# Optimization experiments

Measured on AMD Instinct MI355X. Metric: run time of the kernel, lower is better.

## Reference

```python
import jax, jax.numpy as jnp
import numpy as np

NUM_TOKENS = 8192
HIDDEN = 4096
NUM_EXPERTS = 64
TOP_K = 8


def setup_inputs() -> dict:
    key = jax.random.key(0)
    k1, k2, k3 = jax.random.split(key, 3)
    tokens = jax.random.normal(k1, (NUM_TOKENS, HIDDEN), dtype=jnp.float32)
    token_probs = jax.random.uniform(k2, (NUM_TOKENS, NUM_EXPERTS), dtype=jnp.float32)
    # exactly TOP_K experts per token -> static num_out_tokens
    scores = jax.random.normal(k3, (NUM_TOKENS, NUM_EXPERTS))
    _, topk_idx = jax.lax.top_k(scores, TOP_K)  # [T, K]
    rows = jnp.arange(NUM_TOKENS)[:, None]
    routing_map = jnp.zeros((NUM_TOKENS, NUM_EXPERTS), dtype=bool).at[rows, topk_idx].set(True)
    return {
        "tokens": tokens,
        "token_probs": token_probs,
        "routing_map": routing_map,
        "num_out_tokens": NUM_TOKENS * TOP_K,
    }


def reference(tokens, token_probs, routing_map, num_out_tokens):
    # Fallback (non-fused) path of TurboTokenPermuter.forward.
    num_tokens, _ = tokens.shape
    # routing_map.bool().T -> [E, T]; masked_select in row-major order =
    # for each expert (in order), the token ids routed to it (in token order).
    flat_mask = routing_map.T.reshape(-1)  # [E*T]
    # stable argsort of ~mask puts flat positions of True entries first, in order
    perm = jnp.argsort(~flat_mask, stable=True)[:num_out_tokens]  # flat E*T indices
    sorted_indices = (perm % num_tokens).astype(jnp.int32)  # token ids (column index)
    permuted_probs = token_probs.T.reshape(-1)[perm]
    permuted_input = tokens[sorted_indices]  # index_select along dim 0
    return permuted_input, permuted_probs, sorted_indices
```

## Files before the change

kernel.cpp:

```cpp
#include <hip/hip_runtime.h>
#include <stdint.h>

#define NTOK   8192
#define NEXP   64
#define HID    4096
#define TOPK   8
#define OUTROW 65536
#define CHUNK  256
#define NCHUNK (NTOK / CHUNK)
#define NPART  (NEXP * NCHUNK)

typedef float f32x4 __attribute__((ext_vector_type(4)));

__global__ void pcount_kernel(const int* __restrict__ map, int* __restrict__ pcnt,
                              int* __restrict__ tok_cnt) {
    int b = blockIdx.x;
    int e = b >> 5, c = b & (NCHUNK - 1);
    int lane = threadIdx.x;
    int cnt = 0;
#pragma unroll
    for (int it = 0; it < CHUNK / 64; ++it) {
        int t = c * CHUNK + it * 64 + lane;
        cnt += __popcll(__ballot(map[(size_t)t * NEXP + e] != 0));
    }
    if (lane == 0) pcnt[b] = cnt;
    if (lane < NTOK / NPART) tok_cnt[b * (NTOK / NPART) + lane] = 0;
}

__global__ void assign_kernel(const int* __restrict__ map,
                              const float* __restrict__ probs,
                              const int* __restrict__ pcnt,
                              int* __restrict__ tok_cnt,
                              int* __restrict__ tok_pos,
                              float* __restrict__ probs_out,
                              float* __restrict__ idx_out) {
    int b = blockIdx.x;
    int e = b >> 5, c = b & (NCHUNK - 1);
    int tid = threadIdx.x;
    int w = tid >> 6, lane = tid & 63;

    __shared__ int red[256];
    __shared__ int wcnt[4];

    int acc = 0;
    for (int i = tid; i < b; i += 256) acc += pcnt[i];
    red[tid] = acc;
    __syncthreads();
    for (int off = 128; off > 0; off >>= 1) {
        if (tid < off) red[tid] += red[tid + off];
        __syncthreads();
    }
    int base = red[0];

    int t = c * CHUNK + w * 64 + lane;
    bool m = map[(size_t)t * NEXP + e] != 0;
    unsigned long long bal = __ballot(m);
    int rank = __popcll(bal & ((1ull << lane) - 1ull));
    if (lane == 0) wcnt[w] = __popcll(bal);
    __syncthreads();
    int wbase = 0;
#pragma unroll
    for (int i = 0; i < 4; ++i) wbase += (i < w) ? wcnt[i] : 0;

    if (m) {
        int pos = base + wbase + rank;
        idx_out[pos] = (float)t;
        probs_out[pos] = probs[(size_t)t * NEXP + e];
        int slot = atomicAdd(&tok_cnt[t], 1);
        if (slot < TOPK) tok_pos[t * TOPK + slot] = pos;
    }
}

__global__ void gather_kernel(const float* __restrict__ tokens,
                              const int* __restrict__ tok_pos,
                              float* __restrict__ out_rows) {
    int t = blockIdx.x;
    int tid = threadIdx.x;
    __shared__ int pos_s[TOPK];
    if (tid < TOPK) pos_s[tid] = tok_pos[t * TOPK + tid];
    __syncthreads();

    const f32x4* sp = (const f32x4*)(tokens + (size_t)t * HID);
    f32x4 v0 = __builtin_nontemporal_load(sp + tid);
    f32x4 v1 = __builtin_nontemporal_load(sp + tid + 256);
    f32x4 v2 = __builtin_nontemporal_load(sp + tid + 512);
    f32x4 v3 = __builtin_nontemporal_load(sp + tid + 768);

#pragma unroll
    for (int j = 0; j < TOPK; ++j) {
        unsigned p = (unsigned)pos_s[j];
        if (p >= OUTROW) continue;
        f32x4* dp = (f32x4*)(out_rows + (size_t)p * HID);
        __builtin_nontemporal_store(v0, dp + tid);
        __builtin_nontemporal_store(v1, dp + tid + 256);
        __builtin_nontemporal_store(v2, dp + tid + 512);
        __builtin_nontemporal_store(v3, dp + tid + 768);
    }
}

extern "C" void kernel_launch(void* const* d_in, const int* in_sizes, int n_in,
                              void* d_out, int out_size, void* d_ws, size_t ws_size,
                              hipStream_t stream) {
    const float* tokens = (const float*)d_in[0];
    const float* probs  = (const float*)d_in[1];
    const int*   map    = (const int*)d_in[2];

    float* out_rows  = (float*)d_out;
    float* out_probs = out_rows + (size_t)OUTROW * HID;
    float* out_idx   = out_probs + OUTROW;

    int* pcnt    = (int*)d_ws;
    int* tok_cnt = pcnt + NPART;
    int* tok_pos = tok_cnt + NTOK;

    pcount_kernel<<<NPART, 64, 0, stream>>>(map, pcnt, tok_cnt);
    assign_kernel<<<NPART, CHUNK, 0, stream>>>(map, probs, pcnt, tok_cnt, tok_pos,
                                               out_probs, out_idx);
    gather_kernel<<<NTOK, 256, 0, stream>>>(tokens, tok_pos, out_rows);
}
```

Measured before the change: 268.1 us.

## Pack routing map into per-token bitmasks and compute slots without atomics

The first kernel now reads the routing map row-wise with coalesced loads and ballots each token's 64 expert flags into a 64-bit mask, stored to workspace by the expert-0 blocks. Per-partition counts come from those masks. The assign kernel reads the compact masks instead of strided map entries, and derives each token's output slot by popcount of lower experts rather than an atomic counter, so slots are ordered by expert. The gather kernel drops the shared-memory staging and nontemporal loads/stores in favour of plain accesses. Each of the 2048 count blocks now reads a full 256x64 map chunk instead of one column, which multiplies redundant map traffic. Only expert-0 blocks write the masks, with no cross-block dependency inside that kernel.

```diff
diff --git a/kernel.cpp b/kernel.cpp
--- a/kernel.cpp
+++ b/kernel.cpp
@@ -7,30 +7,44 @@
 #define TOPK   8
 #define OUTROW 65536
 #define CHUNK  256
-#define NCHUNK (NTOK / CHUNK)
-#define NPART  (NEXP * NCHUNK)
+#define NCHUNK 32
+#define NPART  2048
 
 typedef float f32x4 __attribute__((ext_vector_type(4)));
+typedef unsigned long long u64;
 
-__global__ void pcount_kernel(const int* __restrict__ map, int* __restrict__ pcnt,
-                              int* __restrict__ tok_cnt) {
+__global__ void mask_count_kernel(const int* __restrict__ map,
+                                  u64* __restrict__ masks,
+                                  int* __restrict__ pcnt) {
     int b = blockIdx.x;
     int e = b >> 5, c = b & (NCHUNK - 1);
-    int lane = threadIdx.x;
-    int cnt = 0;
-#pragma unroll
-    for (int it = 0; it < CHUNK / 64; ++it) {
-        int t = c * CHUNK + it * 64 + lane;
-        cnt += __popcll(__ballot(map[(size_t)t * NEXP + e] != 0));
+    int tid = threadIdx.x;
+    int w = tid >> 6, lane = tid & 63;
+
+    __shared__ u64 sm[CHUNK];
+    int t0 = c * CHUNK + w * 64;
+#pragma unroll 8
+    for (int i = 0; i < 64; ++i) {
+        int v = map[(size_t)(t0 + i) * NEXP + lane];
+        u64 bal = __ballot(v != 0);
+        if (lane == 0) sm[w * 64 + i] = bal;
     }
-    if (lane == 0) pcnt[b] = cnt;
-    if (lane < NTOK / NPART) tok_cnt[b * (NTOK / NPART) + lane] = 0;
+    __syncthreads();
+    if (e == 0) masks[c * CHUNK + tid] = sm[tid];
+
+    __shared__ int red[256];
+    red[tid] = (int)((sm[tid] >> e) & 1ull);
+    __syncthreads();
+    for (int off = 128; off > 0; off >>= 1) {
+        if (tid < off) red[tid] += red[tid + off];
+        __syncthreads();
+    }
+    if (tid == 0) pcnt[b] = red[0];
 }
 
-__global__ void assign_kernel(const int* __restrict__ map,
+__global__ void assign_kernel(const u64* __restrict__ masks,
                               const float* __restrict__ probs,
                               const int* __restrict__ pcnt,
-                              int* __restrict__ tok_cnt,
                               int* __restrict__ tok_pos,
                               float* __restrict__ probs_out,
                               float* __restrict__ idx_out) {
@@ -52,9 +66,10 @@
     }
     int base = red[0];
 
-    int t = c * CHUNK + w * 64 + lane;
-    bool m = map[(size_t)t * NEXP + e] != 0;
-    unsigned long long bal = __ballot(m);
+    int t = c * CHUNK + tid;
+    u64 mk = masks[t];
+    bool m = (mk >> e) & 1ull;
+    u64 bal = __ballot(m);
     int rank = __popcll(bal & ((1ull << lane) - 1ull));
     if (lane == 0) wcnt[w] = __popcll(bal);
     __syncthreads();
@@ -66,7 +81,7 @@
         int pos = base + wbase + rank;
         idx_out[pos] = (float)t;
         probs_out[pos] = probs[(size_t)t * NEXP + e];
-        int slot = atomicAdd(&tok_cnt[t], 1);
+        int slot = __popcll(mk & ((1ull << e) - 1ull));
         if (slot < TOPK) tok_pos[t * TOPK + slot] = pos;
     }
 }
@@ -76,25 +91,20 @@
                               float* __restrict__ out_rows) {
     int t = blockIdx.x;
     int tid = threadIdx.x;
-    __shared__ int pos_s[TOPK];
-    if (tid < TOPK) pos_s[tid] = tok_pos[t * TOPK + tid];
-    __syncthreads();
-
     const f32x4* sp = (const f32x4*)(tokens + (size_t)t * HID);
-    f32x4 v0 = __builtin_nontemporal_load(sp + tid);
-    f32x4 v1 = __builtin_nontemporal_load(sp + tid + 256);
-    f32x4 v2 = __builtin_nontemporal_load(sp + tid + 512);
-    f32x4 v3 = __builtin_nontemporal_load(sp + tid + 768);
-
+    f32x4 v0 = sp[tid];
+    f32x4 v1 = sp[tid + 256];
+    f32x4 v2 = sp[tid + 512];
+    f32x4 v3 = sp[tid + 768];
 #pragma unroll
     for (int j = 0; j < TOPK; ++j) {
-        unsigned p = (unsigned)pos_s[j];
+        unsigned p = (unsigned)tok_pos[t * TOPK + j];
         if (p >= OUTROW) continue;
         f32x4* dp = (f32x4*)(out_rows + (size_t)p * HID);
-        __builtin_nontemporal_store(v0, dp + tid);
-        __builtin_nontemporal_store(v1, dp + tid + 256);
-        __builtin_nontemporal_store(v2, dp + tid + 512);
-        __builtin_nontemporal_store(v3, dp + tid + 768);
+        dp[tid]       = v0;
+        dp[tid + 256] = v1;
+        dp[tid + 512] = v2;
+        dp[tid + 768] = v3;
     }
 }
 
@@ -109,12 +119,12 @@
     float* out_probs = out_rows + (size_t)OUTROW * HID;
     float* out_idx   = out_probs + OUTROW;
 
-    int* pcnt    = (int*)d_ws;
-    int* tok_cnt = pcnt + NPART;
-    int* tok_pos = tok_cnt + NTOK;
+    u64* masks   = (u64*)d_ws;
+    int* pcnt    = (int*)(masks + NTOK);
+    int* tok_pos = pcnt + NPART;
 
-    pcount_kernel<<<NPART, 64, 0, stream>>>(map, pcnt, tok_cnt);
-    assign_kernel<<<NPART, CHUNK, 0, stream>>>(map, probs, pcnt, tok_cnt, tok_pos,
-                                               out_probs, out_idx);
+    mask_count_kernel<<<NPART, 256, 0, stream>>>(map, masks, pcnt);
+    assign_kernel<<<NPART, 256, 0, stream>>>(masks, probs, pcnt, tok_pos,
+                                             out_probs, out_idx);
     gather_kernel<<<NTOK, 256, 0, stream>>>(tokens, tok_pos, out_rows);
 }
```

Measured after the change: 277.8 us. +3.6%, slower.
